# Kernel optimization log

Hardware: AMD Instinct MI355X
Metric: run time of the kernel (lower is better)

## Reference

```python
import jax, jax.numpy as jnp
import numpy as np

N_NODES = 50000
N_EDGES = 800000
D = 128


def setup_inputs() -> dict:
    key = jax.random.key(0)
    k1, k2, k3, k4 = jax.random.split(key, 4)
    feat = jax.random.normal(k1, (N_NODES, D), dtype=jnp.float32)
    W = jax.random.normal(k2, (D, D), dtype=jnp.float32) * (1.0 / np.sqrt(D))
    b = jnp.zeros((D,), dtype=jnp.float32)
    eps = jnp.zeros((1,), dtype=jnp.float32)
    src = jax.random.randint(k3, (N_EDGES,), 0, N_NODES, dtype=jnp.int64 if jax.config.jax_enable_x64 else jnp.int32)
    dst = jax.random.randint(k4, (N_EDGES,), 0, N_NODES, dtype=jnp.int64 if jax.config.jax_enable_x64 else jnp.int32)
    return {"feat": feat, "W": W, "b": b, "eps": eps, "src": src, "dst": dst}


def reference(feat, W, b, eps, src, dst):
    # message passing: m_e = feat[src_e]; neigh_i = sum_{e: dst_e = i} m_e
    msgs = feat[src]  # [E, D] gather
    neigh = jax.ops.segment_sum(msgs, dst, num_segments=N_NODES)  # [N, D]
    # eps-weighted residual: (1 + eps) * h_dst + neigh
    rst = (1.0 + eps) * feat + neigh  # eps is [1], broadcasts
    # apply_func: Dense(D)
    out = jnp.einsum('nd,de->ne', rst, W) + b
    return out
```

## Files before the change

kernel.cpp:

```cpp
#include <hip/hip_runtime.h>

#define D 128
#define CAP 32
#define OCAP 4096
#define TILE 16

typedef __attribute__((ext_vector_type(8))) short bf16x8;
typedef __attribute__((ext_vector_type(4))) float f32x4;

static __device__ inline short f2bf(float f) {
  union { float f; unsigned u; } v; v.f = f;
  unsigned r = v.u + 0x7FFF + ((v.u >> 16) & 1);
  return (short)(r >> 16);
}
static __device__ inline float bf_lo(unsigned u) {
  union { unsigned u; float f; } v; v.u = u << 16; return v.f;
}
static __device__ inline float bf_hi(unsigned u) {
  union { unsigned u; float f; } v; v.u = u & 0xFFFF0000u; return v.f;
}

static __device__ inline void wfrag_build_one(const float* __restrict__ W,
                                              uint4* __restrict__ wfrag, int t) {
  int c = t >> 8, h = (t >> 6) & 3, l = t & 63;
  int col = c * 16 + (l & 15);
  int k0 = h * 32 + (l >> 4) * 8;
  unsigned u[4];
  #pragma unroll
  for (int p = 0; p < 4; ++p) {
    unsigned lo = (unsigned short)f2bf(W[(k0 + 2 * p) * D + col]);
    unsigned hi = (unsigned short)f2bf(W[(k0 + 2 * p + 1) * D + col]);
    u[p] = lo | (hi << 16);
  }
  wfrag[t] = make_uint4(u[0], u[1], u[2], u[3]);
}

__global__ __launch_bounds__(256) void build_kernel(
    const int* __restrict__ src, const int* __restrict__ dst,
    int* __restrict__ cnt, int* __restrict__ ocount, unsigned* __restrict__ oflow,
    unsigned short* __restrict__ permfix,
    const float* __restrict__ W, uint4* __restrict__ wfrag,
    const float* __restrict__ feat, uint4* __restrict__ featbf,
    int E, int ND8) {
  int grp = blockIdx.x & 7;
  int e = (blockIdx.x >> 3) * 256 + threadIdx.x;
  if (e < E) {
    int d = dst[e];
    if (((d >> 5) & 7) == grp) {
      int s = src[e];
      int c = atomicAdd(&cnt[d], 1);
      if (c < CAP) {
        permfix[(size_t)d * CAP + c] = (unsigned short)s;
      } else {
        int o = atomicAdd(ocount, 1);
        if (o < OCAP) oflow[o] = ((unsigned)d << 16) | (unsigned)s;
      }
    }
  }
  int i = blockIdx.x * 256 + threadIdx.x;
  if (i < ND8) {
    float4 u = ((const float4*)feat)[2 * i];
    float4 v = ((const float4*)feat)[2 * i + 1];
    unsigned w0 = (unsigned short)f2bf(u.x) | ((unsigned)(unsigned short)f2bf(u.y) << 16);
    unsigned w1 = (unsigned short)f2bf(u.z) | ((unsigned)(unsigned short)f2bf(u.w) << 16);
    unsigned w2 = (unsigned short)f2bf(v.x) | ((unsigned)(unsigned short)f2bf(v.y) << 16);
    unsigned w3 = (unsigned short)f2bf(v.z) | ((unsigned)(unsigned short)f2bf(v.w) << 16);
    featbf[i] = make_uint4(w0, w1, w2, w3);
  }
  if (i < 2048) wfrag_build_one(W, wfrag, i);
}

__global__ __launch_bounds__(128, 8) void fused_gather_gemm(
    const uint2* __restrict__ featbf, const float* __restrict__ eps,
    const float* __restrict__ bias, const int* __restrict__ cnt,
    const int* __restrict__ ocount, const unsigned* __restrict__ oflow,
    const unsigned short* __restrict__ permfix,
    const uint4* __restrict__ wfrag, float* __restrict__ out, int N) {
  __shared__ float xs[TILE][132];
  __shared__ float sbias[128];
  __shared__ int scnt[TILE];
  int tid = threadIdx.x;
  int base = blockIdx.x * TILE;
  sbias[tid] = bias[tid];
  if (tid < TILE) {
    int grow = base + tid;
    scnt[tid] = (grow < N) ? cnt[grow] : 0;
  }
  float scale = 1.0f + eps[0];
  __syncthreads();

  int g = tid >> 5, lane = tid & 31;
  for (int it = 0; it < TILE / 4; ++it) {
    int lr = it * 4 + g;
    int grow = base + lr;
    float4 acc = make_float4(0.f, 0.f, 0.f, 0.f);
    if (grow < N) {
      uint2 a0 = featbf[(size_t)grow * 32 + lane];
      acc.x = scale * bf_lo(a0.x);
      acc.y = scale * bf_hi(a0.x);
      acc.z = scale * bf_lo(a0.y);
      acc.w = scale * bf_hi(a0.y);
      int deg = scnt[lr];
      deg = (deg < CAP) ? deg : CAP;
      const unsigned short* pf = permfix + (size_t)grow * CAP;
      int j = 0;
      for (; j + 8 <= deg; j += 8) {
        uint4 pv = *(const uint4*)&pf[j];
        int s0 = pv.x & 0xFFFF, s1 = pv.x >> 16;
        int s2 = pv.y & 0xFFFF, s3 = pv.y >> 16;
        int s4 = pv.z & 0xFFFF, s5 = pv.z >> 16;
        int s6 = pv.w & 0xFFFF, s7 = pv.w >> 16;
        uint2 r0 = featbf[(size_t)s0 * 32 + lane];
        uint2 r1 = featbf[(size_t)s1 * 32 + lane];
        uint2 r2 = featbf[(size_t)s2 * 32 + lane];
        uint2 r3 = featbf[(size_t)s3 * 32 + lane];
        uint2 r4 = featbf[(size_t)s4 * 32 + lane];
        uint2 r5 = featbf[(size_t)s5 * 32 + lane];
        uint2 r6 = featbf[(size_t)s6 * 32 + lane];
        uint2 r7 = featbf[(size_t)s7 * 32 + lane];
        acc.x += bf_lo(r0.x) + bf_lo(r1.x) + bf_lo(r2.x) + bf_lo(r3.x)
               + bf_lo(r4.x) + bf_lo(r5.x) + bf_lo(r6.x) + bf_lo(r7.x);
        acc.y += bf_hi(r0.x) + bf_hi(r1.x) + bf_hi(r2.x) + bf_hi(r3.x)
               + bf_hi(r4.x) + bf_hi(r5.x) + bf_hi(r6.x) + bf_hi(r7.x);
        acc.z += bf_lo(r0.y) + bf_lo(r1.y) + bf_lo(r2.y) + bf_lo(r3.y)
               + bf_lo(r4.y) + bf_lo(r5.y) + bf_lo(r6.y) + bf_lo(r7.y);
        acc.w += bf_hi(r0.y) + bf_hi(r1.y) + bf_hi(r2.y) + bf_hi(r3.y)
               + bf_hi(r4.y) + bf_hi(r5.y) + bf_hi(r6.y) + bf_hi(r7.y);
      }
      if (j + 4 <= deg) {
        uint2 pv = *(const uint2*)&pf[j];
        int s0 = pv.x & 0xFFFF, s1 = pv.x >> 16;
        int s2 = pv.y & 0xFFFF, s3 = pv.y >> 16;
        uint2 r0 = featbf[(size_t)s0 * 32 + lane];
        uint2 r1 = featbf[(size_t)s1 * 32 + lane];
        uint2 r2 = featbf[(size_t)s2 * 32 + lane];
        uint2 r3 = featbf[(size_t)s3 * 32 + lane];
        acc.x += bf_lo(r0.x) + bf_lo(r1.x) + bf_lo(r2.x) + bf_lo(r3.x);
        acc.y += bf_hi(r0.x) + bf_hi(r1.x) + bf_hi(r2.x) + bf_hi(r3.x);
        acc.z += bf_lo(r0.y) + bf_lo(r1.y) + bf_lo(r2.y) + bf_lo(r3.y);
        acc.w += bf_hi(r0.y) + bf_hi(r1.y) + bf_hi(r2.y) + bf_hi(r3.y);
        j += 4;
      }
      for (; j < deg; ++j) {
        uint2 a = featbf[(size_t)pf[j] * 32 + lane];
        acc.x += bf_lo(a.x); acc.y += bf_hi(a.x);
        acc.z += bf_lo(a.y); acc.w += bf_hi(a.y);
      }
    }
    *(float4*)&xs[lr][lane * 4] = acc;
  }
  __syncthreads();

  int novf = *ocount;
  novf = (novf < OCAP) ? novf : OCAP;
  if (novf > 0) {
    if (tid < 32) {
      for (int o = 0; o < novf; ++o) {
        unsigned e = oflow[o];
        int d = (int)(e >> 16);
        if ((d / TILE) == (int)blockIdx.x) {
          int s = (int)(e & 0xFFFF);
          uint2 a = featbf[(size_t)s * 32 + tid];
          int r = d % TILE;
          xs[r][tid * 4 + 0] += bf_lo(a.x);
          xs[r][tid * 4 + 1] += bf_hi(a.x);
          xs[r][tid * 4 + 2] += bf_lo(a.y);
          xs[r][tid * 4 + 3] += bf_hi(a.y);
        }
      }
    }
    __syncthreads();
  }

  int w = tid >> 6;
  int l = tid & 63;
  int rowg = l >> 4, rl = l & 15;
  int cb = w * 4;

  bf16x8 a[4];
  #pragma unroll
  for (int h = 0; h < 4; ++h) {
    const float* p = &xs[rl][h * 32 + rowg * 8];
    float4 u = *(const float4*)p;
    float4 v = *(const float4*)(p + 4);
    bf16x8 t;
    t[0] = f2bf(u.x); t[1] = f2bf(u.y); t[2] = f2bf(u.z); t[3] = f2bf(u.w);
    t[4] = f2bf(v.x); t[5] = f2bf(v.y); t[6] = f2bf(v.z); t[7] = f2bf(v.w);
    a[h] = t;
  }

  const bf16x8* wf = (const bf16x8*)wfrag;
  #pragma unroll
  for (int cl = 0; cl < 4; ++cl) {
    int c = cb + cl;
    float bb = sbias[c * 16 + rl];
    f32x4 acc = {bb, bb, bb, bb};
    #pragma unroll
    for (int h = 0; h < 4; ++h) {
      bf16x8 b = wf[(c * 4 + h) * 64 + l];
      acc = __builtin_amdgcn_mfma_f32_16x16x32_bf16(a[h], b, acc, 0, 0, 0);
    }
    #pragma unroll
    for (int r = 0; r < 4; ++r) {
      int row = base + rowg * 4 + r;
      if (row < N) out[(size_t)row * D + c * 16 + rl] = acc[r];
    }
  }
}

__global__ __launch_bounds__(256) void init_out_kernel(
    const float* __restrict__ feat, const float* __restrict__ eps,
    float* __restrict__ out, int n4) {
  int i = blockIdx.x * blockDim.x + threadIdx.x;
  if (i >= n4) return;
  float scale = 1.0f + eps[0];
  float4 v = ((const float4*)feat)[i];
  v.x *= scale; v.y *= scale; v.z *= scale; v.w *= scale;
  ((float4*)out)[i] = v;
}

__global__ __launch_bounds__(256) void scatter_add_kernel(
    const float* __restrict__ feat, const int* __restrict__ src,
    const int* __restrict__ dst, float* __restrict__ out, int E) {
  int gid = blockIdx.x * blockDim.x + threadIdx.x;
  int e = gid >> 5;
  int lane = gid & 31;
  if (e >= E) return;
  int s = src[e], d = dst[e];
  float4 v = ((const float4*)(feat + (size_t)s * D))[lane];
  float* o = out + (size_t)d * D + lane * 4;
  unsafeAtomicAdd(o + 0, v.x);
  unsafeAtomicAdd(o + 1, v.y);
  unsafeAtomicAdd(o + 2, v.z);
  unsafeAtomicAdd(o + 3, v.w);
}

#define ROWS 64
__global__ __launch_bounds__(256) void gemm_inplace_kernel(
    float* __restrict__ out, const float* __restrict__ Wm,
    const float* __restrict__ bias, int N) {
  __shared__ float Ws[D * D];
  __shared__ float xs[ROWS * D];
  int tid = threadIdx.x;
  int base = blockIdx.x * ROWS;
  #pragma unroll
  for (int it = 0; it < 16; ++it) {
    int idx = tid + 256 * it;
    ((float4*)Ws)[idx] = ((const float4*)Wm)[idx];
  }
  #pragma unroll
  for (int it = 0; it < 8; ++it) {
    int idx = tid + 256 * it;
    int row = idx >> 5, c4 = idx & 31;
    float4 v = make_float4(0.f, 0.f, 0.f, 0.f);
    if (base + row < N) v = ((const float4*)(out + (size_t)(base + row) * D))[c4];
    ((float4*)xs)[row * 32 + c4] = v;
  }
  __syncthreads();
  int tc = tid & 31, tr = tid >> 5;
  float acc[8][4];
  #pragma unroll
  for (int r = 0; r < 8; ++r)
    #pragma unroll
    for (int i = 0; i < 4; ++i) acc[r][i] = 0.f;
  for (int k0 = 0; k0 < D; k0 += 4) {
    float4 f[8];
    #pragma unroll
    for (int r = 0; r < 8; ++r) f[r] = *(const float4*)&xs[(tr * 8 + r) * D + k0];
    float w[4][4];
    #pragma unroll
    for (int u = 0; u < 4; ++u)
      #pragma unroll
      for (int i = 0; i < 4; ++i) w[u][i] = Ws[(k0 + u) * D + tc + 32 * i];
    #pragma unroll
    for (int r = 0; r < 8; ++r)
      #pragma unroll
      for (int i = 0; i < 4; ++i) {
        acc[r][i] += f[r].x * w[0][i];
        acc[r][i] += f[r].y * w[1][i];
        acc[r][i] += f[r].z * w[2][i];
        acc[r][i] += f[r].w * w[3][i];
      }
  }
  float bv[4];
  #pragma unroll
  for (int i = 0; i < 4; ++i) bv[i] = bias[tc + 32 * i];
  #pragma unroll
  for (int r = 0; r < 8; ++r) {
    int row = base + tr * 8 + r;
    if (row < N) {
      #pragma unroll
      for (int i = 0; i < 4; ++i)
        out[(size_t)row * D + tc + 32 * i] = acc[r][i] + bv[i];
    }
  }
}

extern "C" void kernel_launch(void* const* d_in, const int* in_sizes, int n_in,
                              void* d_out, int out_size, void* d_ws, size_t ws_size,
                              hipStream_t stream) {
  const float* feat = (const float*)d_in[0];
  const float* Wm   = (const float*)d_in[1];
  const float* bias = (const float*)d_in[2];
  const float* eps  = (const float*)d_in[3];
  const int*   src  = (const int*)d_in[4];
  const int*   dst  = (const int*)d_in[5];
  float* out = (float*)d_out;

  int N = in_sizes[0] / D;
  int E = in_sizes[4];
  int ND8 = (N * D) / 8;

  size_t cnt_b    = (size_t)N * 4;
  size_t ocount_b = 4;
  size_t oflow_b  = (size_t)OCAP * 4;
  size_t perm_b   = (size_t)N * CAP * 2;
  size_t wfrag_off = (cnt_b + ocount_b + oflow_b + perm_b + 15) & ~(size_t)15;
  size_t featbf_off = wfrag_off + 2048 * 16;
  size_t needed = featbf_off + (size_t)N * D * 2;

  if (ws_size >= needed) {
    int* cnt = (int*)d_ws;
    int* ocount = cnt + N;
    unsigned* oflow = (unsigned*)(ocount + 1);
    unsigned short* permfix = (unsigned short*)(oflow + OCAP);
    uint4* wfrag = (uint4*)((char*)d_ws + wfrag_off);
    uint4* featbf = (uint4*)((char*)d_ws + featbf_off);

    hipMemsetAsync(cnt, 0, cnt_b + ocount_b, stream);

    int chunks = (E + 255) / 256;
    build_kernel<<<8 * chunks, 256, 0, stream>>>(
        src, dst, cnt, ocount, oflow, permfix, Wm, wfrag, feat, featbf, E, ND8);

    fused_gather_gemm<<<(N + TILE - 1) / TILE, 128, 0, stream>>>(
        (const uint2*)featbf, eps, bias, cnt, ocount, oflow, permfix, wfrag, out, N);
  } else {
    int n4 = (N * D) / 4;
    init_out_kernel<<<(n4 + 255) / 256, 256, 0, stream>>>(feat, eps, out, n4);
    long long total_threads = (long long)E * 32;
    int sblocks = (int)((total_threads + 255) / 256);
    scatter_add_kernel<<<sblocks, 256, 0, stream>>>(feat, src, dst, out, E);
    int gblocks2 = (N + ROWS - 1) / ROWS;
    gemm_inplace_kernel<<<gblocks2, 256, 0, stream>>>(out, Wm, bias, N);
  }
}
```

Before: 92.64 us.

## Pack per-node count and neighbor list into one 64-byte bucket line

Merges the per-destination edge counter and its 16-bit source list into a single 64-byte line per node (a 4-byte count followed by 30 slots). The gather kernel reads the whole line with four vector loads, which drops the separate count array, the shared-memory count staging and one barrier. The unrolled add8 blocks now take their indices straight from registers. In exchange the memset grows from 4 to 64 bytes per node, capacity falls from 32 to 30 so more edges spill to the overflow path, and the trailing barrier now runs unconditionally.

```diff
diff --git a/kernel.cpp b/kernel.cpp
--- a/kernel.cpp
+++ b/kernel.cpp
@@ -1,7 +1,7 @@
 #include <hip/hip_runtime.h>
 
 #define D 128
-#define CAP 32
+#define CAP 30
 #define OCAP 4096
 #define TILE 16
 
@@ -37,8 +37,8 @@
 
 __global__ __launch_bounds__(256) void build_kernel(
     const int* __restrict__ src, const int* __restrict__ dst,
-    int* __restrict__ cnt, int* __restrict__ ocount, unsigned* __restrict__ oflow,
-    unsigned short* __restrict__ permfix,
+    unsigned short* __restrict__ bkt, int* __restrict__ ocount,
+    unsigned* __restrict__ oflow,
     const float* __restrict__ W, uint4* __restrict__ wfrag,
     const float* __restrict__ feat, uint4* __restrict__ featbf,
     int E, int ND8) {
@@ -48,9 +48,10 @@
     int d = dst[e];
     if (((d >> 5) & 7) == grp) {
       int s = src[e];
-      int c = atomicAdd(&cnt[d], 1);
+      unsigned* line = (unsigned*)(bkt + (size_t)d * 32);
+      unsigned c = atomicAdd(line, 1u);
       if (c < CAP) {
-        permfix[(size_t)d * CAP + c] = (unsigned short)s;
+        ((unsigned short*)line)[2 + c] = (unsigned short)s;
       } else {
         int o = atomicAdd(ocount, 1);
         if (o < OCAP) oflow[o] = ((unsigned)d << 16) | (unsigned)s;
@@ -70,24 +71,42 @@
   if (i < 2048) wfrag_build_one(W, wfrag, i);
 }
 
+static __device__ inline void add8(unsigned w0, unsigned w1, unsigned w2, unsigned w3,
+                                   const uint2* __restrict__ featbf, int lane,
+                                   float4& acc) {
+  int s0 = w0 & 0xFFFF, s1 = w0 >> 16;
+  int s2 = w1 & 0xFFFF, s3 = w1 >> 16;
+  int s4 = w2 & 0xFFFF, s5 = w2 >> 16;
+  int s6 = w3 & 0xFFFF, s7 = w3 >> 16;
+  uint2 r0 = featbf[(size_t)s0 * 32 + lane];
+  uint2 r1 = featbf[(size_t)s1 * 32 + lane];
+  uint2 r2 = featbf[(size_t)s2 * 32 + lane];
+  uint2 r3 = featbf[(size_t)s3 * 32 + lane];
+  uint2 r4 = featbf[(size_t)s4 * 32 + lane];
+  uint2 r5 = featbf[(size_t)s5 * 32 + lane];
+  uint2 r6 = featbf[(size_t)s6 * 32 + lane];
+  uint2 r7 = featbf[(size_t)s7 * 32 + lane];
+  acc.x += bf_lo(r0.x) + bf_lo(r1.x) + bf_lo(r2.x) + bf_lo(r3.x)
+         + bf_lo(r4.x) + bf_lo(r5.x) + bf_lo(r6.x) + bf_lo(r7.x);
+  acc.y += bf_hi(r0.x) + bf_hi(r1.x) + bf_hi(r2.x) + bf_hi(r3.x)
+         + bf_hi(r4.x) + bf_hi(r5.x) + bf_hi(r6.x) + bf_hi(r7.x);
+  acc.z += bf_lo(r0.y) + bf_lo(r1.y) + bf_lo(r2.y) + bf_lo(r3.y)
+         + bf_lo(r4.y) + bf_lo(r5.y) + bf_lo(r6.y) + bf_lo(r7.y);
+  acc.w += bf_hi(r0.y) + bf_hi(r1.y) + bf_hi(r2.y) + bf_hi(r3.y)
+         + bf_hi(r4.y) + bf_hi(r5.y) + bf_hi(r6.y) + bf_hi(r7.y);
+}
+
 __global__ __launch_bounds__(128, 8) void fused_gather_gemm(
     const uint2* __restrict__ featbf, const float* __restrict__ eps,
-    const float* __restrict__ bias, const int* __restrict__ cnt,
+    const float* __restrict__ bias, const unsigned short* __restrict__ bkt,
     const int* __restrict__ ocount, const unsigned* __restrict__ oflow,
-    const unsigned short* __restrict__ permfix,
     const uint4* __restrict__ wfrag, float* __restrict__ out, int N) {
   __shared__ float xs[TILE][132];
   __shared__ float sbias[128];
-  __shared__ int scnt[TILE];
   int tid = threadIdx.x;
   int base = blockIdx.x * TILE;
   sbias[tid] = bias[tid];
-  if (tid < TILE) {
-    int grow = base + tid;
-    scnt[tid] = (grow < N) ? cnt[grow] : 0;
-  }
   float scale = 1.0f + eps[0];
-  __syncthreads();
 
   int g = tid >> 5, lane = tid & 31;
   for (int it = 0; it < TILE / 4; ++it) {
@@ -95,54 +114,34 @@
     int grow = base + lr;
     float4 acc = make_float4(0.f, 0.f, 0.f, 0.f);
     if (grow < N) {
+      const uint4* bl = (const uint4*)(bkt + (size_t)grow * 32);
+      uint4 q0 = bl[0];
+      uint4 q1 = bl[1];
+      uint4 q2 = bl[2];
+      uint4 q3 = bl[3];
       uint2 a0 = featbf[(size_t)grow * 32 + lane];
       acc.x = scale * bf_lo(a0.x);
       acc.y = scale * bf_hi(a0.x);
       acc.z = scale * bf_lo(a0.y);
       acc.w = scale * bf_hi(a0.y);
-      int deg = scnt[lr];
+      int deg = (int)q0.x;
       deg = (deg < CAP) ? deg : CAP;
-      const unsigned short* pf = permfix + (size_t)grow * CAP;
       int j = 0;
-      for (; j + 8 <= deg; j += 8) {
-        uint4 pv = *(const uint4*)&pf[j];
-        int s0 = pv.x & 0xFFFF, s1 = pv.x >> 16;
-        int s2 = pv.y & 0xFFFF, s3 = pv.y >> 16;
-        int s4 = pv.z & 0xFFFF, s5 = pv.z >> 16;
-        int s6 = pv.w & 0xFFFF, s7 = pv.w >> 16;
-        uint2 r0 = featbf[(size_t)s0 * 32 + lane];
-        uint2 r1 = featbf[(size_t)s1 * 32 + lane];
-        uint2 r2 = featbf[(size_t)s2 * 32 + lane];
-        uint2 r3 = featbf[(size_t)s3 * 32 + lane];
-        uint2 r4 = featbf[(size_t)s4 * 32 + lane];
-        uint2 r5 = featbf[(size_t)s5 * 32 + lane];
-        uint2 r6 = featbf[(size_t)s6 * 32 + lane];
-        uint2 r7 = featbf[(size_t)s7 * 32 + lane];
-        acc.x += bf_lo(r0.x) + bf_lo(r1.x) + bf_lo(r2.x) + bf_lo(r3.x)
-               + bf_lo(r4.x) + bf_lo(r5.x) + bf_lo(r6.x) + bf_lo(r7.x);
-        acc.y += bf_hi(r0.x) + bf_hi(r1.x) + bf_hi(r2.x) + bf_hi(r3.x)
-               + bf_hi(r4.x) + bf_hi(r5.x) + bf_hi(r6.x) + bf_hi(r7.x);
-        acc.z += bf_lo(r0.y) + bf_lo(r1.y) + bf_lo(r2.y) + bf_lo(r3.y)
-               + bf_lo(r4.y) + bf_lo(r5.y) + bf_lo(r6.y) + bf_lo(r7.y);
-        acc.w += bf_hi(r0.y) + bf_hi(r1.y) + bf_hi(r2.y) + bf_hi(r3.y)
-               + bf_hi(r4.y) + bf_hi(r5.y) + bf_hi(r6.y) + bf_hi(r7.y);
-      }
-      if (j + 4 <= deg) {
-        uint2 pv = *(const uint2*)&pf[j];
-        int s0 = pv.x & 0xFFFF, s1 = pv.x >> 16;
-        int s2 = pv.y & 0xFFFF, s3 = pv.y >> 16;
-        uint2 r0 = featbf[(size_t)s0 * 32 + lane];
-        uint2 r1 = featbf[(size_t)s1 * 32 + lane];
-        uint2 r2 = featbf[(size_t)s2 * 32 + lane];
-        uint2 r3 = featbf[(size_t)s3 * 32 + lane];
-        acc.x += bf_lo(r0.x) + bf_lo(r1.x) + bf_lo(r2.x) + bf_lo(r3.x);
-        acc.y += bf_hi(r0.x) + bf_hi(r1.x) + bf_hi(r2.x) + bf_hi(r3.x);
-        acc.z += bf_lo(r0.y) + bf_lo(r1.y) + bf_lo(r2.y) + bf_lo(r3.y);
-        acc.w += bf_hi(r0.y) + bf_hi(r1.y) + bf_hi(r2.y) + bf_hi(r3.y);
-        j += 4;
-      }
+      if (deg >= 8) {
+        add8(q0.y, q0.z, q0.w, q1.x, featbf, lane, acc);
+        j = 8;
+        if (deg >= 16) {
+          add8(q1.y, q1.z, q1.w, q2.x, featbf, lane, acc);
+          j = 16;
+          if (deg >= 24) {
+            add8(q2.y, q2.z, q2.w, q3.x, featbf, lane, acc);
+            j = 24;
+          }
+        }
+      }
+      const unsigned short* hs = (const unsigned short*)bl;
       for (; j < deg; ++j) {
-        uint2 a = featbf[(size_t)pf[j] * 32 + lane];
+        uint2 a = featbf[(size_t)hs[2 + j] * 32 + lane];
         acc.x += bf_lo(a.x); acc.y += bf_hi(a.x);
         acc.z += bf_lo(a.y); acc.w += bf_hi(a.y);
       }
@@ -169,8 +168,8 @@
         }
       }
     }
-    __syncthreads();
-  }
+  }
+  __syncthreads();
 
   int w = tid >> 6;
   int l = tid & 63;
@@ -311,30 +310,27 @@
   int E = in_sizes[4];
   int ND8 = (N * D) / 8;
 
-  size_t cnt_b    = (size_t)N * 4;
-  size_t ocount_b = 4;
-  size_t oflow_b  = (size_t)OCAP * 4;
-  size_t perm_b   = (size_t)N * CAP * 2;
-  size_t wfrag_off = (cnt_b + ocount_b + oflow_b + perm_b + 15) & ~(size_t)15;
+  size_t bkt_b   = (size_t)N * 64;
+  size_t oflow_off = bkt_b + 4;
+  size_t wfrag_off = (oflow_off + (size_t)OCAP * 4 + 15) & ~(size_t)15;
   size_t featbf_off = wfrag_off + 2048 * 16;
   size_t needed = featbf_off + (size_t)N * D * 2;
 
   if (ws_size >= needed) {
-    int* cnt = (int*)d_ws;
-    int* ocount = cnt + N;
-    unsigned* oflow = (unsigned*)(ocount + 1);
-    unsigned short* permfix = (unsigned short*)(oflow + OCAP);
+    unsigned short* bkt = (unsigned short*)d_ws;
+    int* ocount = (int*)((char*)d_ws + bkt_b);
+    unsigned* oflow = (unsigned*)((char*)d_ws + oflow_off);
     uint4* wfrag = (uint4*)((char*)d_ws + wfrag_off);
     uint4* featbf = (uint4*)((char*)d_ws + featbf_off);
 
-    hipMemsetAsync(cnt, 0, cnt_b + ocount_b, stream);
+    hipMemsetAsync(bkt, 0, bkt_b + 4, stream);
 
     int chunks = (E + 255) / 256;
     build_kernel<<<8 * chunks, 256, 0, stream>>>(
-        src, dst, cnt, ocount, oflow, permfix, Wm, wfrag, feat, featbf, E, ND8);
+        src, dst, bkt, ocount, oflow, Wm, wfrag, feat, featbf, E, ND8);
 
     fused_gather_gemm<<<(N + TILE - 1) / TILE, 128, 0, stream>>>(
-        (const uint2*)featbf, eps, bias, cnt, ocount, oflow, permfix, wfrag, out, N);
+        (const uint2*)featbf, eps, bias, bkt, ocount, oflow, wfrag, out, N);
   } else {
     int n4 = (N * D) / 4;
     init_out_kernel<<<(n4 + 255) / 256, 256, 0, stream>>>(feat, eps, out, n4);
```

After: 148.6 us. 60.4% more time.
